# Optimization experiments

Hardware: AMD Instinct MI355X
Metric: run time of the kernel (lower is better)

The kernel has to match this reference:

```python
import jax, jax.numpy as jnp
import numpy as np

N = 50000      # nodes
E = 400000     # edges (before self-loops)
IN = 128       # input feature dim
HID = 32       # out_channels per head
HEADS = 12
NC = 2         # num_classes
SLOPE = 0.2    # GATv2 leaky_relu negative slope


def setup_inputs() -> dict:
    key = jax.random.key(0)
    ks = jax.random.split(key, 24)
    f32 = jnp.float32
    def nrm(k, shape, s=0.1):
        return jax.random.normal(k, shape, dtype=f32) * s
    inp = {}
    inp["x"] = jax.random.normal(ks[0], (N, IN), dtype=f32)
    inp["edge_index"] = jax.random.randint(ks[1], (2, E), 0, N, dtype=jnp.int32)
    # GATv2 layer 0: in=IN, layer 1: in=HID; both heads=HEADS, out=HID, concat=False
    dims = [IN, HID]
    i = 2
    for l, d in enumerate(dims):
        inp[f"Wl{l}"] = nrm(ks[i], (d, HEADS * HID)); i += 1
        inp[f"bl{l}"] = jnp.zeros((HEADS * HID,), f32)
        inp[f"Wr{l}"] = nrm(ks[i], (d, HEADS * HID)); i += 1
        inp[f"br{l}"] = jnp.zeros((HEADS * HID,), f32)
        inp[f"att{l}"] = nrm(ks[i], (HEADS, HID)); i += 1
        inp[f"bias{l}"] = jnp.zeros((HID,), f32)
    # output GATv2Conv(HID, NC): heads=1, concat=True
    inp["Wlo"] = nrm(ks[i], (HID, NC)); i += 1
    inp["blo"] = jnp.zeros((NC,), f32)
    inp["Wro"] = nrm(ks[i], (HID, NC)); i += 1
    inp["bro"] = jnp.zeros((NC,), f32)
    inp["atto"] = nrm(ks[i], (1, NC)); i += 1
    inp["biaso"] = jnp.zeros((NC,), f32)
    return inp


def gatv2_conv(x, src, dst, Wl, bl, Wr, br, att, bias, heads, out_ch, concat):
    """PyG GATv2Conv (share_weights=False, self-loops pre-appended, eval mode)."""
    n = x.shape[0]
    xl = (x @ Wl + bl).reshape(n, heads, out_ch)   # source transform
    xr = (x @ Wr + br).reshape(n, heads, out_ch)   # target transform
    # per-edge attention: e_ij = att . leaky_relu(xl_j + xr_i)
    h = jax.nn.leaky_relu(xl[src] + xr[dst], SLOPE)            # [E, H, C]
    logits = jnp.einsum('ehc,hc->eh', h, att)                   # [E, H]
    # segment softmax over incoming edges per destination node
    m = jax.ops.segment_max(logits, dst, num_segments=n)        # [N, H]
    a = jnp.exp(logits - m[dst])
    denom = jax.ops.segment_sum(a, dst, num_segments=n)         # [N, H]
    alpha = a / (denom[dst] + 1e-16)                            # [E, H]
    out = jax.ops.segment_sum(xl[src] * alpha[..., None], dst, num_segments=n)
    out = out.reshape(n, heads * out_ch) if concat else out.mean(axis=1)
    return out + bias


def reference(x, edge_index, Wl0, bl0, Wr0, br0, att0, bias0,
              Wl1, bl1, Wr1, br1, att1, bias1,
              Wlo, blo, Wro, bro, atto, biaso):
    n = x.shape[0]
    loop = jnp.arange(n, dtype=edge_index.dtype)
    src = jnp.concatenate([edge_index[0], loop])  # add self-loops (PyG default)
    dst = jnp.concatenate([edge_index[1], loop])
    h = gatv2_conv(x, src, dst, Wl0, bl0, Wr0, br0, att0, bias0, HEADS, HID, False)
    h = jax.nn.elu(h)
    h = gatv2_conv(h, src, dst, Wl1, bl1, Wr1, br1, att1, bias1, HEADS, HID, False)
    h = jax.nn.elu(h)
    out = gatv2_conv(h, src, dst, Wlo, blo, Wro, bro, atto, biaso, 1, NC, True)
    return out
```

## Files before the change

### kernel.cpp

```cpp
#include <hip/hip_runtime.h>
#include <hip/hip_fp16.h>
#include <math.h>

#define IN_DIM 128
#define HID 32
#define HEADS 12
#define FDIM (HEADS*HID)
#define SLOPE 0.2f

typedef __attribute__((ext_vector_type(8))) short short8;
typedef __attribute__((ext_vector_type(4))) float float4v;
typedef __attribute__((ext_vector_type(4))) float f32x4;
typedef _Float16 hv2 __attribute__((ext_vector_type(2)));

__device__ __forceinline__ float dot2acc(hv2 a, hv2 b, float c) {
#if __has_builtin(__builtin_amdgcn_fdot2)
    return __builtin_amdgcn_fdot2(a, b, c, false);
#else
    return c + (float)a.x * (float)b.x + (float)a.y * (float)b.y;
#endif
}


__global__ void hist_kernel(const int* __restrict__ dst, int* __restrict__ cnt, int E) {
    int e = blockIdx.x * blockDim.x + threadIdx.x;
    if (e < E) atomicAdd(&cnt[dst[e]], 1);
}

__global__ __launch_bounds__(256) void scan_partial_kernel(const int* __restrict__ cnt,
                                                           int* __restrict__ partials, int n) {
    int i = blockIdx.x * 256 + threadIdx.x;
    int v = (i < n) ? cnt[i] : 0;
#pragma unroll
    for (int off = 1; off < 64; off <<= 1) v += __shfl_xor(v, off);
    __shared__ int sh[4];
    if ((threadIdx.x & 63) == 0) sh[threadIdx.x >> 6] = v;
    __syncthreads();
    if (threadIdx.x == 0) partials[blockIdx.x] = sh[0] + sh[1] + sh[2] + sh[3];
}

__global__ __launch_bounds__(1024) void scan_top_kernel(int* __restrict__ partials, int nb) {
    __shared__ int sh[1024];
    int t = threadIdx.x;
    int v = (t < nb) ? partials[t] : 0;
    sh[t] = v;
    __syncthreads();
    for (int off = 1; off < 1024; off <<= 1) {
        int u = (t >= off) ? sh[t - off] : 0;
        __syncthreads();
        sh[t] += u;
        __syncthreads();
    }
    if (t < nb) partials[t] = sh[t] - v;
}

__global__ __launch_bounds__(256) void scan_final_kernel(const int* __restrict__ cnt,
                                                         const int* __restrict__ partials,
                                                         int* __restrict__ start,
                                                         int* __restrict__ cursor, int n) {
    __shared__ int sh[256];
    int t = threadIdx.x;
    int i = blockIdx.x * 256 + t;
    int v = (i < n) ? cnt[i] : 0;
    sh[t] = v;
    __syncthreads();
    for (int off = 1; off < 256; off <<= 1) {
        int u = (t >= off) ? sh[t - off] : 0;
        __syncthreads();
        sh[t] += u;
        __syncthreads();
    }
    int ex = sh[t] - v + partials[blockIdx.x];
    if (i < n) {
        start[i] = ex;
        cursor[i] = ex;
        if (i == n - 1) start[n] = ex + v;
    }
}

__global__ void scatter_kernel(const int* __restrict__ src, const int* __restrict__ dst,
                               int* __restrict__ cursor, int* __restrict__ srcs,
                               int* __restrict__ srcsOff, int E) {
    int e = blockIdx.x * blockDim.x + threadIdx.x;
    if (e < E) {
        int d = dst[e];
        int pos = atomicAdd(&cursor[d], 1);
        int s = src[e];
        srcs[pos] = s;
        srcsOff[pos] = s * (FDIM * 2);
    }
}


__device__ __forceinline__ unsigned int bf16_rne(float f) {
    unsigned int u = __float_as_uint(f);
    return (u + 0x7FFFu + ((u >> 16) & 1u)) >> 16;
}


__global__ void prep_all(const float* __restrict__ Wl0, const float* __restrict__ Wr0,
                         const float* __restrict__ Wl1, const float* __restrict__ Wr1,
                         const float* __restrict__ a0, const float* __restrict__ a1,
                         short* __restrict__ Bl0h, short* __restrict__ Bl0l,
                         short* __restrict__ Br0h, short* __restrict__ Br0l,
                         short* __restrict__ Bl1h, short* __restrict__ Bl1l,
                         short* __restrict__ Br1h, short* __restrict__ Br1l,
                         _Float16* __restrict__ attH) {
    int idx = blockIdx.x * 256 + threadIdx.x;
    if (idx < 49152) {
        int k = idx / 384, n = idx - k * 384;
        float w1 = Wl0[idx], w2 = Wr0[idx];
        unsigned int h1 = bf16_rne(w1);
        unsigned int l1 = bf16_rne(w1 - __uint_as_float(h1 << 16));
        unsigned int h2 = bf16_rne(w2);
        unsigned int l2 = bf16_rne(w2 - __uint_as_float(h2 << 16));
        Bl0h[n * 128 + k] = (short)h1;  Bl0l[n * 128 + k] = (short)l1;
        Br0h[n * 128 + k] = (short)h2;  Br0l[n * 128 + k] = (short)l2;
    } else if (idx < 61440) {
        int i2 = idx - 49152;
        int k = i2 / 384, n = i2 - k * 384;
        float w1 = Wl1[i2], w2 = Wr1[i2];
        unsigned int h1 = bf16_rne(w1);
        unsigned int l1 = bf16_rne(w1 - __uint_as_float(h1 << 16));
        unsigned int h2 = bf16_rne(w2);
        unsigned int l2 = bf16_rne(w2 - __uint_as_float(h2 << 16));
        Bl1h[n * 32 + k] = (short)h1;  Bl1l[n * 32 + k] = (short)l1;
        Br1h[n * 32 + k] = (short)h2;  Br1l[n * 32 + k] = (short)l2;
    } else if (idx < 62208) {
        int i2 = idx - 61440;
        attH[i2] = (_Float16)((i2 < 384) ? a0[i2] : a1[i2 - 384]);
    }
}


__global__ __launch_bounds__(256) void gemm_pair_mfma_f32A(
    const float* __restrict__ A,
    const short* __restrict__ B1h, const short* __restrict__ B1l,
    const float* __restrict__ bias1, __half* __restrict__ C1,
    const short* __restrict__ B2h, const short* __restrict__ B2l,
    const float* __restrict__ bias2, __half* __restrict__ C2,
    int M, int K) {
    __shared__ __align__(16) unsigned char smem[33792];
    uint4* AsHi = (uint4*)smem;
    uint4* AsLo = AsHi + 512;
    uint4* BsHi = AsLo + 512;
    uint4* BsLo = BsHi + 512;
    int tid = threadIdx.x;
    int lane = tid & 63;
    int wave = tid >> 6;
    int wm = wave & 1, wn = wave >> 1;
    int rowBase = blockIdx.x * 128;
    bool second = blockIdx.y >= 3;
    int colBase = (blockIdx.y - (second ? 3 : 0)) * 128;
    const short* Bh  = second ? B2h : B1h;
    const short* Bl  = second ? B2l : B1l;
    const float* bias = second ? bias2 : bias1;
    __half*      C    = second ? C2 : C1;

    float4v acc[4][4];
#pragma unroll
    for (int i = 0; i < 4; i++)
#pragma unroll
        for (int j = 0; j < 4; j++) acc[i][j] = (float4v){0.f, 0.f, 0.f, 0.f};

    for (int kt = 0; kt < K; kt += 32) {
#pragma unroll
        for (int i = 0; i < 2; i++) {
            int c = i * 256 + tid;
            int o = c >> 7, r = c & 127;
            int gr = rowBase + r;
            float4 f0 = make_float4(0.f, 0.f, 0.f, 0.f), f1 = f0;
            if (gr < M) {
                const float* p = A + (size_t)gr * K + kt + o * 8;
                f0 = *(const float4*)p;
                f1 = *(const float4*)(p + 4);
            }
            float fs[8] = {f0.x, f0.y, f0.z, f0.w, f1.x, f1.y, f1.z, f1.w};
            unsigned int hb[8], lb[8];
#pragma unroll
            for (int t = 0; t < 8; t++) {
                hb[t] = bf16_rne(fs[t]);
                lb[t] = bf16_rne(fs[t] - __uint_as_float(hb[t] << 16));
            }
            uint4 hi, lo;
            hi.x = hb[0] | (hb[1] << 16); hi.y = hb[2] | (hb[3] << 16);
            hi.z = hb[4] | (hb[5] << 16); hi.w = hb[6] | (hb[7] << 16);
            lo.x = lb[0] | (lb[1] << 16); lo.y = lb[2] | (lb[3] << 16);
            lo.z = lb[4] | (lb[5] << 16); lo.w = lb[6] | (lb[7] << 16);
            int slot = (r >> 4) * 64 + (o << 4) + (r & 15);
            AsHi[slot] = hi;
            AsLo[slot] = lo;
        }
#pragma unroll
        for (int i = 0; i < 4; i++) {
            int c = i * 256 + tid;
            int h = c >> 9, o = (c >> 7) & 3, n = c & 127;
            const short* src = h ? Bl : Bh;
            uint4 v = *(const uint4*)(src + (size_t)(colBase + n) * K + kt + o * 8);
            int slot = (n >> 4) * 64 + (o << 4) + (n & 15);
            if (h) BsLo[slot] = v; else BsHi[slot] = v;
        }
        __syncthreads();

        short8 ah[4], al[4], bh[4], blv[4];
#pragma unroll
        for (int i = 0; i < 4; i++) {
            ah[i]  = ((const short8*)AsHi)[(wm * 4 + i) * 64 + lane];
            al[i]  = ((const short8*)AsLo)[(wm * 4 + i) * 64 + lane];
            bh[i]  = ((const short8*)BsHi)[(wn * 4 + i) * 64 + lane];
            blv[i] = ((const short8*)BsLo)[(wn * 4 + i) * 64 + lane];
        }
#pragma unroll
        for (int i = 0; i < 4; i++)
#pragma unroll
            for (int j = 0; j < 4; j++) {
                acc[i][j] = __builtin_amdgcn_mfma_f32_16x16x32_bf16(ah[i], bh[j],  acc[i][j], 0, 0, 0);
                acc[i][j] = __builtin_amdgcn_mfma_f32_16x16x32_bf16(ah[i], blv[j], acc[i][j], 0, 0, 0);
                acc[i][j] = __builtin_amdgcn_mfma_f32_16x16x32_bf16(al[i], bh[j],  acc[i][j], 0, 0, 0);
            }
        __syncthreads();
    }

    float* Ct = (float*)smem;
    int cq = lane >> 4, cn = lane & 15;
#pragma unroll
    for (int ph = 0; ph < 2; ph++) {
        if (wm == ph) {
#pragma unroll
            for (int i = 0; i < 4; i++)
#pragma unroll
                for (int j = 0; j < 4; j++) {
                    int lr = i * 16 + cq * 4;
                    int lc = wn * 64 + j * 16 + cn;
#pragma unroll
                    for (int r = 0; r < 4; r++)
                        Ct[(lr + r) * 132 + lc] = acc[i][j][r];
                }
        }
        __syncthreads();
#pragma unroll
        for (int k = 0; k < 4; k++) {
            int o = k * 256 + tid;
            int lr = o >> 4;
            int oc = (o & 15) << 3;
            int gr = rowBase + ph * 64 + lr;
            if (gr < M) {
                float4 f0 = *(float4*)&Ct[lr * 132 + oc];
                float4 f1 = *(float4*)&Ct[lr * 132 + oc + 4];
                int gc = colBase + oc;
                float4 b0 = *(const float4*)(bias + gc);
                float4 b1 = *(const float4*)(bias + gc + 4);
                __half2 p0 = __floats2half2_rn(f0.x + b0.x, f0.y + b0.y);
                __half2 p1 = __floats2half2_rn(f0.z + b0.z, f0.w + b0.w);
                __half2 p2 = __floats2half2_rn(f1.x + b1.x, f1.y + b1.y);
                __half2 p3 = __floats2half2_rn(f1.z + b1.z, f1.w + b1.w);
                uint4 ov;
                ov.x = *(unsigned int*)&p0;
                ov.y = *(unsigned int*)&p1;
                ov.z = *(unsigned int*)&p2;
                ov.w = *(unsigned int*)&p3;
                *(uint4*)(C + (size_t)gr * FDIM + gc) = ov;
            }
        }
        __syncthreads();
    }
}


__global__ __launch_bounds__(256) void gemm_pair_mfma_preA(
    const short* __restrict__ Ahi, const short* __restrict__ Alo,
    const short* __restrict__ B1h, const short* __restrict__ B1l,
    const float* __restrict__ bias1, __half* __restrict__ C1,
    const short* __restrict__ B2h, const short* __restrict__ B2l,
    const float* __restrict__ bias2, __half* __restrict__ C2,
    int M, int K) {
    __shared__ __align__(16) unsigned char smem[33792];
    uint4* AsHi = (uint4*)smem;
    uint4* AsLo = AsHi + 512;
    uint4* BsHi = AsLo + 512;
    uint4* BsLo = BsHi + 512;
    int tid = threadIdx.x;
    int lane = tid & 63;
    int wave = tid >> 6;
    int wm = wave & 1, wn = wave >> 1;
    int rowBase = blockIdx.x * 128;
    bool second = blockIdx.y >= 3;
    int colBase = (blockIdx.y - (second ? 3 : 0)) * 128;
    const short* Bh  = second ? B2h : B1h;
    const short* Bl  = second ? B2l : B1l;
    const float* bias = second ? bias2 : bias1;
    __half*      C    = second ? C2 : C1;

    float4v acc[4][4];
#pragma unroll
    for (int i = 0; i < 4; i++)
#pragma unroll
        for (int j = 0; j < 4; j++) acc[i][j] = (float4v){0.f, 0.f, 0.f, 0.f};

    for (int kt = 0; kt < K; kt += 32) {
#pragma unroll
        for (int i = 0; i < 2; i++) {
            int c = i * 256 + tid;
            int o = c >> 7, r = c & 127;
            int gr = rowBase + r;
            uint4 hv = make_uint4(0, 0, 0, 0), lv = hv;
            if (gr < M) {
                hv = *(const uint4*)(Ahi + (size_t)gr * K + kt + o * 8);
                lv = *(const uint4*)(Alo + (size_t)gr * K + kt + o * 8);
            }
            int slot = (r >> 4) * 64 + (o << 4) + (r & 15);
            AsHi[slot] = hv;
            AsLo[slot] = lv;
        }
#pragma unroll
        for (int i = 0; i < 4; i++) {
            int c = i * 256 + tid;
            int h = c >> 9, o = (c >> 7) & 3, n = c & 127;
            const short* src = h ? Bl : Bh;
            uint4 v = *(const uint4*)(src + (size_t)(colBase + n) * K + kt + o * 8);
            int slot = (n >> 4) * 64 + (o << 4) + (n & 15);
            if (h) BsLo[slot] = v; else BsHi[slot] = v;
        }
        __syncthreads();

        short8 ah[4], al[4], bh[4], blv[4];
#pragma unroll
        for (int i = 0; i < 4; i++) {
            ah[i]  = ((const short8*)AsHi)[(wm * 4 + i) * 64 + lane];
            al[i]  = ((const short8*)AsLo)[(wm * 4 + i) * 64 + lane];
            bh[i]  = ((const short8*)BsHi)[(wn * 4 + i) * 64 + lane];
            blv[i] = ((const short8*)BsLo)[(wn * 4 + i) * 64 + lane];
        }
#pragma unroll
        for (int i = 0; i < 4; i++)
#pragma unroll
            for (int j = 0; j < 4; j++) {
                acc[i][j] = __builtin_amdgcn_mfma_f32_16x16x32_bf16(ah[i], bh[j],  acc[i][j], 0, 0, 0);
                acc[i][j] = __builtin_amdgcn_mfma_f32_16x16x32_bf16(ah[i], blv[j], acc[i][j], 0, 0, 0);
                acc[i][j] = __builtin_amdgcn_mfma_f32_16x16x32_bf16(al[i], bh[j],  acc[i][j], 0, 0, 0);
            }
        __syncthreads();
    }

    float* Ct = (float*)smem;
    int cq = lane >> 4, cn = lane & 15;
#pragma unroll
    for (int ph = 0; ph < 2; ph++) {
        if (wm == ph) {
#pragma unroll
            for (int i = 0; i < 4; i++)
#pragma unroll
                for (int j = 0; j < 4; j++) {
                    int lr = i * 16 + cq * 4;
                    int lc = wn * 64 + j * 16 + cn;
#pragma unroll
                    for (int r = 0; r < 4; r++)
                        Ct[(lr + r) * 132 + lc] = acc[i][j][r];
                }
        }
        __syncthreads();
#pragma unroll
        for (int k = 0; k < 4; k++) {
            int o = k * 256 + tid;
            int lr = o >> 4;
            int oc = (o & 15) << 3;
            int gr = rowBase + ph * 64 + lr;
            if (gr < M) {
                float4 f0 = *(float4*)&Ct[lr * 132 + oc];
                float4 f1 = *(float4*)&Ct[lr * 132 + oc + 4];
                int gc = colBase + oc;
                float4 b0 = *(const float4*)(bias + gc);
                float4 b1 = *(const float4*)(bias + gc + 4);
                __half2 p0 = __floats2half2_rn(f0.x + b0.x, f0.y + b0.y);
                __half2 p1 = __floats2half2_rn(f0.z + b0.z, f0.w + b0.w);
                __half2 p2 = __floats2half2_rn(f1.x + b1.x, f1.y + b1.y);
                __half2 p3 = __floats2half2_rn(f1.z + b1.z, f1.w + b1.w);
                uint4 ov;
                ov.x = *(unsigned int*)&p0;
                ov.y = *(unsigned int*)&p1;
                ov.z = *(unsigned int*)&p2;
                ov.w = *(unsigned int*)&p3;
                *(uint4*)(C + (size_t)gr * FDIM + gc) = ov;
            }
        }
        __syncthreads();
    }
}


__global__ __launch_bounds__(256) void agg_kernel(const __half* __restrict__ xl,
                                                  const __half* __restrict__ xr,
                                                  const _Float16* __restrict__ att_h,
                                                  const float* __restrict__ bias,
                                                  const int* __restrict__ start,
                                                  const int* __restrict__ srcsOff,
                                                  short* __restrict__ houtHi,
                                                  short* __restrict__ houtLo,
                                                  const float* __restrict__ Wl,
                                                  const float* __restrict__ bl,
                                                  const float* __restrict__ Wr,
                                                  const float* __restrict__ br,
                                                  float* __restrict__ xloB,
                                                  float* __restrict__ xroB, int N) {
    int node = (blockIdx.x << 2) + (threadIdx.x >> 6);
    if (node >= N) return;
    int lane = threadIdx.x & 63;
    int hl = lane & 31;
    int half_ = lane >> 5;
    int cb = hl << 3;

    long nodeOff = (long)node * (FDIM * 2);
    hv2 xr2[6], at2[6];
    f32x4 acc[3];
    float s[3];
#pragma unroll
    for (int c = 0; c < 3; c++) {
        uint2 ur = *(const uint2*)((const char*)xr + nodeOff + c * 256 + cb);
        xr2[2*c]   = __builtin_bit_cast(hv2, ur.x);
        xr2[2*c+1] = __builtin_bit_cast(hv2, ur.y);
        uint2 ua = *(const uint2*)((const char*)att_h + c * 256 + cb);
        at2[2*c]   = __builtin_bit_cast(hv2, ua.x);
        at2[2*c+1] = __builtin_bit_cast(hv2, ua.y);
        acc[c] = (f32x4){0.f, 0.f, 0.f, 0.f};
        s[c] = 0.f;
    }
    const hv2 sl2 = {(_Float16)SLOPE, (_Float16)SLOPE};
    const char* xlb = (const char*)xl;

    int e0 = start[node], e1 = start[node + 1];

    for (int b = e0 - 1; b < e1; b += 4) {
        hv2 xa[2][6];
        float mask[2];
#pragma unroll
        for (int p = 0; p < 2; p++) {
            int myIdx = b + p * 2 + half_;
            int ic = min(myIdx, e1 - 1);
            long off = (ic < e0) ? nodeOff : (long)srcsOff[ic];
            mask[p] = (myIdx < e1) ? 0.f : -1e30f;
            const char* base = xlb + off + cb;
            uint2 u0 = *(const uint2*)(base);
            uint2 u1 = *(const uint2*)(base + 256);
            uint2 u2 = *(const uint2*)(base + 512);
            xa[p][0] = __builtin_bit_cast(hv2, u0.x); xa[p][1] = __builtin_bit_cast(hv2, u0.y);
            xa[p][2] = __builtin_bit_cast(hv2, u1.x); xa[p][3] = __builtin_bit_cast(hv2, u1.y);
            xa[p][4] = __builtin_bit_cast(hv2, u2.x); xa[p][5] = __builtin_bit_cast(hv2, u2.y);
        }
#pragma unroll
        for (int p = 0; p < 2; p++) {
            float pc[3];
#pragma unroll
            for (int c = 0; c < 3; c++) {
                hv2 t0 = xa[p][2*c]   + xr2[2*c];
                hv2 t1 = xa[p][2*c+1] + xr2[2*c+1];
                t0 = __builtin_elementwise_max(t0, t0 * sl2);
                t1 = __builtin_elementwise_max(t1, t1 * sl2);
                pc[c] = dot2acc(t1, at2[2*c+1], dot2acc(t0, at2[2*c], 0.f));
            }
#pragma unroll
            for (int st = 1; st <= 4; st <<= 1) {
                pc[0] += __shfl_xor(pc[0], st);
                pc[1] += __shfl_xor(pc[1], st);
                pc[2] += __shfl_xor(pc[2], st);
            }
#pragma unroll
            for (int c = 0; c < 3; c++) {
                float a = __expf(pc[c] + mask[p]);
                s[c] += a;
                acc[c].x = fmaf(a, (float)xa[p][2*c].x,   acc[c].x);
                acc[c].y = fmaf(a, (float)xa[p][2*c].y,   acc[c].y);
                acc[c].z = fmaf(a, (float)xa[p][2*c+1].x, acc[c].z);
                acc[c].w = fmaf(a, (float)xa[p][2*c+1].y, acc[c].w);
            }
        }
    }

#pragma unroll
    for (int c = 0; c < 3; c++) {
        acc[c].x += __shfl_xor(acc[c].x, 32);
        acc[c].y += __shfl_xor(acc[c].y, 32);
        acc[c].z += __shfl_xor(acc[c].z, 32);
        acc[c].w += __shfl_xor(acc[c].w, 32);
        s[c] += __shfl_xor(s[c], 32);
    }
    f32x4 v[3];
#pragma unroll
    for (int c = 0; c < 3; c++) {
        float inv = 1.f / (s[c] + 1e-16f);
        f32x4 iv = {inv, inv, inv, inv};
        v[c] = acc[c] * iv;
    }
#pragma unroll
    for (int st = 8; st <= 16; st <<= 1) {
#pragma unroll
        for (int c = 0; c < 3; c++) {
            v[c].x += __shfl_xor(v[c].x, st);
            v[c].y += __shfl_xor(v[c].y, st);
            v[c].z += __shfl_xor(v[c].z, st);
            v[c].w += __shfl_xor(v[c].w, st);
        }
    }
    if (lane < 8) {
        f32x4 b4 = *(const f32x4*)(bias + (hl << 2));
        f32x4 o = (v[0] + v[1] + v[2]) * (f32x4){1.f/12.f, 1.f/12.f, 1.f/12.f, 1.f/12.f} + b4;
        o.x = o.x > 0.f ? o.x : expm1f(o.x);
        o.y = o.y > 0.f ? o.y : expm1f(o.y);
        o.z = o.z > 0.f ? o.z : expm1f(o.z);
        o.w = o.w > 0.f ? o.w : expm1f(o.w);
        if (houtHi) {
            float fs[4] = {o.x, o.y, o.z, o.w};
            unsigned int hb[4], lb[4];
#pragma unroll
            for (int t = 0; t < 4; t++) {
                hb[t] = bf16_rne(fs[t]);
                lb[t] = bf16_rne(fs[t] - __uint_as_float(hb[t] << 16));
            }
            uint2 hp, lp;
            hp.x = hb[0] | (hb[1] << 16); hp.y = hb[2] | (hb[3] << 16);
            lp.x = lb[0] | (lb[1] << 16); lp.y = lb[2] | (lb[3] << 16);
            *(uint2*)(houtHi + (size_t)node * 32 + (hl << 2)) = hp;
            *(uint2*)(houtLo + (size_t)node * 32 + (hl << 2)) = lp;
        }
        if (Wl) {
            f32x4 wl0 = *(const f32x4*)(Wl + (hl << 3));
            f32x4 wl1 = *(const f32x4*)(Wl + (hl << 3) + 4);
            f32x4 wr0 = *(const f32x4*)(Wr + (hl << 3));
            f32x4 wr1 = *(const f32x4*)(Wr + (hl << 3) + 4);
            float l0 = o.x * wl0.x + o.y * wl0.z + o.z * wl1.x + o.w * wl1.z;
            float l1 = o.x * wl0.y + o.y * wl0.w + o.z * wl1.y + o.w * wl1.w;
            float r0 = o.x * wr0.x + o.y * wr0.z + o.z * wr1.x + o.w * wr1.z;
            float r1 = o.x * wr0.y + o.y * wr0.w + o.z * wr1.y + o.w * wr1.w;
#pragma unroll
            for (int st = 1; st <= 4; st <<= 1) {
                l0 += __shfl_xor(l0, st); l1 += __shfl_xor(l1, st);
                r0 += __shfl_xor(r0, st); r1 += __shfl_xor(r1, st);
            }
            if (hl == 0) {
                xloB[2 * node]     = l0 + bl[0];
                xloB[2 * node + 1] = l1 + bl[1];
                xroB[2 * node]     = r0 + br[0];
                xroB[2 * node + 1] = r1 + br[1];
            }
        }
    }
}


__global__ void out_agg_kernel(const float* __restrict__ xlo, const float* __restrict__ xro,
                               const float* __restrict__ atto, const float* __restrict__ biaso,
                               const int* __restrict__ start, const int* __restrict__ srcs,
                               float* __restrict__ out, int N) {
    int i = blockIdx.x * blockDim.x + threadIdx.x;
    if (i >= N) return;
    float a0 = atto[0], a1 = atto[1];
    float xr0 = xro[2 * i], xr1 = xro[2 * i + 1];
    float s = 0.f, acc0 = 0.f, acc1 = 0.f;
    int e0 = start[i], e1 = start[i + 1];
    for (int idx = e0 - 1; idx < e1; ++idx) {
        int j = (idx < e0) ? i : srcs[idx];
        float x0 = xlo[2 * j], x1 = xlo[2 * j + 1];
        float t0 = x0 + xr0, t1 = x1 + xr1;
        t0 = fmaxf(t0, SLOPE * t0);
        t1 = fmaxf(t1, SLOPE * t1);
        float L = a0 * t0 + a1 * t1;
        float a = __expf(L);
        s += a;
        acc0 = fmaf(a, x0, acc0);
        acc1 = fmaf(a, x1, acc1);
    }
    float inv = 1.0f / (s + 1e-16f);
    out[2 * i]     = acc0 * inv + biaso[0];
    out[2 * i + 1] = acc1 * inv + biaso[1];
}


extern "C" void kernel_launch(void* const* d_in, const int* in_sizes, int n_in,
                              void* d_out, int out_size, void* d_ws, size_t ws_size,
                              hipStream_t stream) {
    const float* x    = (const float*)d_in[0];
    const int*   ei   = (const int*)d_in[1];
    const float* Wl0  = (const float*)d_in[2];
    const float* bl0  = (const float*)d_in[3];
    const float* Wr0  = (const float*)d_in[4];
    const float* br0  = (const float*)d_in[5];
    const float* att0 = (const float*)d_in[6];
    const float* bias0= (const float*)d_in[7];
    const float* Wl1  = (const float*)d_in[8];
    const float* bl1  = (const float*)d_in[9];
    const float* Wr1  = (const float*)d_in[10];
    const float* br1  = (const float*)d_in[11];
    const float* att1 = (const float*)d_in[12];
    const float* bias1= (const float*)d_in[13];
    const float* Wlo  = (const float*)d_in[14];
    const float* blo  = (const float*)d_in[15];
    const float* Wro  = (const float*)d_in[16];
    const float* bro  = (const float*)d_in[17];
    const float* atto = (const float*)d_in[18];
    const float* biaso= (const float*)d_in[19];

    const int N = in_sizes[0] / IN_DIM;
    const int E = in_sizes[1] / 2;

    char* ws = (char*)d_ws;
    size_t off = 0;
    auto take = [&](size_t bytes) -> char* {
        char* p = ws + off;
        off += (bytes + 255) & ~(size_t)255;
        return p;
    };
    __half* xlf = (__half*)take((size_t)N * FDIM * 2);
    __half* xrf = (__half*)take((size_t)N * FDIM * 2);
    float* xloB = (float*)take((size_t)N * 2 * 4);
    float* xroB = (float*)take((size_t)N * 2 * 4);
    int* cnt    = (int*)take((size_t)N * 4);
    int* startA = (int*)take((size_t)(N + 1) * 4);
    int* cursor = (int*)take((size_t)N * 4);
    int* srcs   = (int*)take((size_t)E * 4);
    int* srcsOff= (int*)take((size_t)E * 4);
    int  nb     = (N + 255) / 256;
    int* partials = (int*)take((size_t)nb * 4);
    short* Bl0h = (short*)take((size_t)FDIM * IN_DIM * 2);
    short* Bl0l = (short*)take((size_t)FDIM * IN_DIM * 2);
    short* Br0h = (short*)take((size_t)FDIM * IN_DIM * 2);
    short* Br0l = (short*)take((size_t)FDIM * IN_DIM * 2);
    short* Bl1h = (short*)take((size_t)FDIM * HID * 2);
    short* Bl1l = (short*)take((size_t)FDIM * HID * 2);
    short* Br1h = (short*)take((size_t)FDIM * HID * 2);
    short* Br1l = (short*)take((size_t)FDIM * HID * 2);
    short* h0h  = (short*)take((size_t)N * HID * 2);
    short* h0l  = (short*)take((size_t)N * HID * 2);
    _Float16* attH = (_Float16*)take((size_t)768 * 2);

    const int* esrc = ei;
    const int* edst = ei + E;

    prep_all<<<(62208 + 255) / 256, 256, 0, stream>>>(Wl0, Wr0, Wl1, Wr1, att0, att1,
                                                      Bl0h, Bl0l, Br0h, Br0l,
                                                      Bl1h, Bl1l, Br1h, Br1l, attH);

    hipMemsetAsync(cnt, 0, (size_t)N * 4, stream);
    hist_kernel<<<(E + 255) / 256, 256, 0, stream>>>(edst, cnt, E);
    scan_partial_kernel<<<nb, 256, 0, stream>>>(cnt, partials, N);
    scan_top_kernel<<<1, 1024, 0, stream>>>(partials, nb);
    scan_final_kernel<<<nb, 256, 0, stream>>>(cnt, partials, startA, cursor, N);
    scatter_kernel<<<(E + 255) / 256, 256, 0, stream>>>(esrc, edst, cursor, srcs, srcsOff, E);

    dim3 ggrid((N + 127) / 128, 6);
    gemm_pair_mfma_f32A<<<ggrid, 256, 0, stream>>>(x, Bl0h, Bl0l, bl0, xlf, Br0h, Br0l, br0, xrf, N, IN_DIM);
    agg_kernel<<<(N + 3) / 4, 256, 0, stream>>>(xlf, xrf, attH, bias0, startA, srcsOff,
                                                h0h, h0l, nullptr, nullptr, nullptr, nullptr,
                                                nullptr, nullptr, N);
    gemm_pair_mfma_preA<<<ggrid, 256, 0, stream>>>(h0h, h0l, Bl1h, Bl1l, bl1, xlf, Br1h, Br1l, br1, xrf, N, HID);
    agg_kernel<<<(N + 3) / 4, 256, 0, stream>>>(xlf, xrf, attH + 384, bias1, startA, srcsOff,
                                                nullptr, nullptr, Wlo, blo, Wro, bro,
                                                xloB, xroB, N);
    out_agg_kernel<<<(N + 255) / 256, 256, 0, stream>>>(xloB, xroB, atto, biaso, startA, srcs, (float*)d_out, N);
}
```

Measured before the change: 407.9 us.

## Process nodes in degree-sorted order in aggregation kernels for load balance

Adds a counting sort of nodes by in-degree (histogram, reversed scan, scatter) that builds a permutation with the highest-degree nodes first. The aggregation kernels and the output aggregation then walk nodes through this permutation, so warps and blocks handle nodes of similar degree. This is meant to cut divergence and tail imbalance from uneven degree distributions. The cost is three small extra kernels plus a memset, and output writes become scattered instead of contiguous.

```diff
diff --git a/kernel.cpp b/kernel.cpp
--- a/kernel.cpp
+++ b/kernel.cpp
@@ -88,6 +88,38 @@
         int s = src[e];
         srcs[pos] = s;
         srcsOff[pos] = s * (FDIM * 2);
+    }
+}
+
+
+__global__ void deg_hist_kernel(const int* __restrict__ cnt, int* __restrict__ degHist, int n) {
+    int i = blockIdx.x * blockDim.x + threadIdx.x;
+    if (i < n) atomicAdd(&degHist[min(cnt[i], 255)], 1);
+}
+
+__global__ __launch_bounds__(256) void deg_scan_kernel(const int* __restrict__ degHist,
+                                                       int* __restrict__ degCursor) {
+    __shared__ int sh[256];
+    int t = threadIdx.x;
+    int v = degHist[255 - t];
+    sh[t] = v;
+    __syncthreads();
+    for (int off = 1; off < 256; off <<= 1) {
+        int u = (t >= off) ? sh[t - off] : 0;
+        __syncthreads();
+        sh[t] += u;
+        __syncthreads();
+    }
+    degCursor[255 - t] = sh[t] - v;
+}
+
+__global__ void deg_scatter_kernel(const int* __restrict__ cnt, int* __restrict__ degCursor,
+                                   int* __restrict__ perm, int n) {
+    int i = blockIdx.x * blockDim.x + threadIdx.x;
+    if (i < n) {
+        int d = min(cnt[i], 255);
+        int pos = atomicAdd(&degCursor[d], 1);
+        perm[pos] = i;
     }
 }
 
@@ -394,6 +426,7 @@
                                                   const float* __restrict__ bias,
                                                   const int* __restrict__ start,
                                                   const int* __restrict__ srcsOff,
+                                                  const int* __restrict__ perm,
                                                   short* __restrict__ houtHi,
                                                   short* __restrict__ houtLo,
                                                   const float* __restrict__ Wl,
@@ -402,8 +435,9 @@
                                                   const float* __restrict__ br,
                                                   float* __restrict__ xloB,
                                                   float* __restrict__ xroB, int N) {
-    int node = (blockIdx.x << 2) + (threadIdx.x >> 6);
-    if (node >= N) return;
+    int nidx = (blockIdx.x << 2) + (threadIdx.x >> 6);
+    if (nidx >= N) return;
+    int node = perm[nidx];
     int lane = threadIdx.x & 63;
     int hl = lane & 31;
     int half_ = lane >> 5;
@@ -549,9 +583,11 @@
 __global__ void out_agg_kernel(const float* __restrict__ xlo, const float* __restrict__ xro,
                                const float* __restrict__ atto, const float* __restrict__ biaso,
                                const int* __restrict__ start, const int* __restrict__ srcs,
+                               const int* __restrict__ perm,
                                float* __restrict__ out, int N) {
-    int i = blockIdx.x * blockDim.x + threadIdx.x;
-    if (i >= N) return;
+    int g = blockIdx.x * blockDim.x + threadIdx.x;
+    if (g >= N) return;
+    int i = perm[g];
     float a0 = atto[0], a1 = atto[1];
     float xr0 = xro[2 * i], xr1 = xro[2 * i + 1];
     float s = 0.f, acc0 = 0.f, acc1 = 0.f;
@@ -619,6 +655,9 @@
     int* srcsOff= (int*)take((size_t)E * 4);
     int  nb     = (N + 255) / 256;
     int* partials = (int*)take((size_t)nb * 4);
+    int* degHist  = (int*)take(512 * 4);
+    int* degCursor= degHist + 256;
+    int* perm     = (int*)take((size_t)N * 4);
     short* Bl0h = (short*)take((size_t)FDIM * IN_DIM * 2);
     short* Bl0l = (short*)take((size_t)FDIM * IN_DIM * 2);
     short* Br0h = (short*)take((size_t)FDIM * IN_DIM * 2);
@@ -639,20 +678,24 @@
                                                       Bl1h, Bl1l, Br1h, Br1l, attH);
 
     hipMemsetAsync(cnt, 0, (size_t)N * 4, stream);
+    hipMemsetAsync(degHist, 0, 512 * 4, stream);
     hist_kernel<<<(E + 255) / 256, 256, 0, stream>>>(edst, cnt, E);
     scan_partial_kernel<<<nb, 256, 0, stream>>>(cnt, partials, N);
     scan_top_kernel<<<1, 1024, 0, stream>>>(partials, nb);
     scan_final_kernel<<<nb, 256, 0, stream>>>(cnt, partials, startA, cursor, N);
     scatter_kernel<<<(E + 255) / 256, 256, 0, stream>>>(esrc, edst, cursor, srcs, srcsOff, E);
+    deg_hist_kernel<<<nb, 256, 0, stream>>>(cnt, degHist, N);
+    deg_scan_kernel<<<1, 256, 0, stream>>>(degHist, degCursor);
+    deg_scatter_kernel<<<nb, 256, 0, stream>>>(cnt, degCursor, perm, N);
 
     dim3 ggrid((N + 127) / 128, 6);
     gemm_pair_mfma_f32A<<<ggrid, 256, 0, stream>>>(x, Bl0h, Bl0l, bl0, xlf, Br0h, Br0l, br0, xrf, N, IN_DIM);
-    agg_kernel<<<(N + 3) / 4, 256, 0, stream>>>(xlf, xrf, attH, bias0, startA, srcsOff,
+    agg_kernel<<<(N + 3) / 4, 256, 0, stream>>>(xlf, xrf, attH, bias0, startA, srcsOff, perm,
                                                 h0h, h0l, nullptr, nullptr, nullptr, nullptr,
                                                 nullptr, nullptr, N);
     gemm_pair_mfma_preA<<<ggrid, 256, 0, stream>>>(h0h, h0l, Bl1h, Bl1l, bl1, xlf, Br1h, Br1l, br1, xrf, N, HID);
-    agg_kernel<<<(N + 3) / 4, 256, 0, stream>>>(xlf, xrf, attH + 384, bias1, startA, srcsOff,
+    agg_kernel<<<(N + 3) / 4, 256, 0, stream>>>(xlf, xrf, attH + 384, bias1, startA, srcsOff, perm,
                                                 nullptr, nullptr, Wlo, blo, Wro, bro,
                                                 xloB, xroB, N);
-    out_agg_kernel<<<(N + 255) / 256, 256, 0, stream>>>(xloB, xroB, atto, biaso, startA, srcs, (float*)d_out, N);
-}
+    out_agg_kernel<<<(N + 255) / 256, 256, 0, stream>>>(xloB, xroB, atto, biaso, startA, srcs, perm, (float*)d_out, N);
+}
```

After: 757.0 us. 85.6% more time.
